# Optimization experiments

Hardware: AMD Instinct MI355X
Metric: run time of the kernel (lower is better)

Reference implementation:

```python
import jax, jax.numpy as jnp
import numpy as np

N, D, C = 4096, 512, 100000
S_SCALE, MARGIN = 30.0, 0.4


def setup_inputs() -> dict:
    key = jax.random.key(0)
    k1, k2, k3 = jax.random.split(key, 3)
    x = jax.random.normal(k1, (N, D), dtype=jnp.float32)
    labels = jax.random.randint(k2, (N,), 0, C, dtype=jnp.int64)
    # fc weight [out_features, in_features]; scaled so s*logits stays in fp32 exp range
    W = jax.random.normal(k3, (C, D), dtype=jnp.float32) * 0.02
    return {"x": x, "labels": labels, "W": W}


def reference(x, labels, W):
    # NOTE: the torch weight-normalization loop is a no-op (rebinds a local),
    # so W is used UNNORMALIZED, faithfully matching the executed torch math.
    xn = x / jnp.linalg.norm(x, axis=1, keepdims=True)          # F.normalize(x, dim=1)
    wf = jnp.einsum('nd,cd->nc', xn, W)                          # [N, C] logits
    target = jnp.take_along_axis(wf, labels[:, None], axis=1)[:, 0]  # wf[i, y_i]
    numerator = S_SCALE * (target - MARGIN)
    # sum over j != y_i of exp(s * wf[i, j]) without materializing per-row exclusions
    excl_sum = jnp.sum(jnp.exp(S_SCALE * wf), axis=1) - jnp.exp(S_SCALE * target)
    denominator = jnp.exp(numerator) + excl_sum
    L = numerator - jnp.log(denominator)
    return -jnp.mean(L)
```

## Files before the change

kernel.cpp:

```cpp
#include <hip/hip_runtime.h>

#define N_ROWS 4096
#define D_DIM  512
#define C_CLS  100000
#define S_SCALE 30.0f
#define MARGIN  0.4f

#define KS 16
#define NT 4
#define MTMAX 7
#define NBLK 1024
#define NTILES 6252
#define BASE_MT 6
#define EXTRA_T 108
#define LDS_BYTES (MTMAX * KS * 64 * 16)

typedef __attribute__((ext_vector_type(8))) __bf16 bf16x8;
typedef __attribute__((ext_vector_type(4))) float floatx4;

__device__ inline unsigned int f2bf_rne(float f) {
    unsigned int u = __builtin_bit_cast(unsigned int, f);
    u += 0x7fffu + ((u >> 16) & 1u);
    return u >> 16;
}

__device__ inline uint4 pack_bf16x8(float4 a, float4 b) {
    uint4 r;
    r.x = f2bf_rne(a.x) | (f2bf_rne(a.y) << 16);
    r.y = f2bf_rne(a.z) | (f2bf_rne(a.w) << 16);
    r.z = f2bf_rne(b.x) | (f2bf_rne(b.y) << 16);
    r.w = f2bf_rne(b.z) | (f2bf_rne(b.w) << 16);
    return r;
}

__global__ __launch_bounds__(256) void normalize_pack(
    const float* __restrict__ x, const int* __restrict__ labels,
    const float* __restrict__ W, uint4* __restrict__ xnp, float* __restrict__ target,
    float* __restrict__ row_sum)
{
    const int gt = blockIdx.x * 256 + threadIdx.x;
    if (gt < N_ROWS) row_sum[gt] = 0.f;

    const int lane = threadIdx.x & 63;
    const int r = blockIdx.x * 4 + (threadIdx.x >> 6);
    const float4* xr = (const float4*)(x + (size_t)r * D_DIM);
    float4 a = xr[lane * 2], b = xr[lane * 2 + 1];
    float ss = a.x*a.x + a.y*a.y + a.z*a.z + a.w*a.w
             + b.x*b.x + b.y*b.y + b.z*b.z + b.w*b.w;
    #pragma unroll
    for (int o = 1; o < 64; o <<= 1) ss += __shfl_xor(ss, o, 64);
    const float inv = 1.0f / sqrtf(ss);

    const int lab = labels[r];
    const float4* wr = (const float4*)(W + (size_t)lab * D_DIM);
    float4 wa = wr[lane * 2], wb = wr[lane * 2 + 1];
    float dot = a.x*wa.x + a.y*wa.y + a.z*wa.z + a.w*wa.w
              + b.x*wb.x + b.y*wb.y + b.z*wb.z + b.w*wb.w;
    #pragma unroll
    for (int o = 1; o < 64; o <<= 1) dot += __shfl_xor(dot, o, 64);
    if (lane == 0) target[r] = dot * inv;

    float4 na = {a.x*inv, a.y*inv, a.z*inv, a.w*inv};
    float4 nb = {b.x*inv, b.y*inv, b.z*inv, b.w*inv};
    const int nt = r >> 4, ks = lane >> 2, li = (r & 15) | ((lane & 3) << 4);
    xnp[(size_t)(nt * KS + ks) * 64 + li] = pack_bf16x8(na, nb);
}

__global__ __launch_bounds__(512, 2) void adms_main(
    const float* __restrict__ W, const uint4* __restrict__ xnp, float* __restrict__ row_sum)
{
    extern __shared__ uint4 sW[];
    const int tid = threadIdx.x, bid = blockIdx.x;
    const int tbase = bid * BASE_MT + (bid < EXTRA_T ? bid : EXTRA_T);
    const int cnt   = BASE_MT + (bid < EXTRA_T ? 1 : 0);
    const int c0 = tbase * 16;

    for (int g = tid >> 6; g < cnt * KS; g += 8) {
        const int mt = g >> 4, ks = g & 15;
        const int j8 = tid & 3, lm = (tid >> 2) & 15;
        const int gc = c0 + mt * 16 + lm;
        const int k0 = ks * 32 + j8 * 8;
        float4 v0 = {0.f,0.f,0.f,0.f}, v1 = {0.f,0.f,0.f,0.f};
        if (gc < C_CLS) {
            const float4* src = (const float4*)(W + (size_t)gc * D_DIM + k0);
            v0 = src[0]; v1 = src[1];
        }
        sW[(mt * KS + ks) * 64 + (lm | (j8 << 4))] = pack_bf16x8(v0, v1);
    }
    __syncthreads();

    const int w = tid >> 6, lane = tid & 63;
    const float s_log2e = S_SCALE * 1.44269504088896340736f;

    for (int iter = 0; iter < N_ROWS / 512; ++iter) {
        const int rbase = iter * 512 + w * 64;
        floatx4 acc[MTMAX][NT] = {};
        const size_t b0 = (size_t)(rbase >> 4) * (KS * 64) + lane;

        #pragma unroll 4
        for (int ks = 0; ks < KS; ++ks) {
            uint4 bfr[NT], afr[MTMAX];
            #pragma unroll
            for (int nt = 0; nt < NT; ++nt)
                bfr[nt] = xnp[b0 + (size_t)nt * (KS * 64) + ks * 64];
            #pragma unroll
            for (int mt = 0; mt < MTMAX; ++mt)
                if (mt < cnt) afr[mt] = sW[(mt * KS + ks) * 64 + lane];
            #pragma unroll
            for (int mt = 0; mt < MTMAX; ++mt)
                if (mt < cnt)
                    #pragma unroll
                    for (int nt = 0; nt < NT; ++nt)
                        acc[mt][nt] = __builtin_amdgcn_mfma_f32_16x16x32_bf16(
                            __builtin_bit_cast(bf16x8, afr[mt]),
                            __builtin_bit_cast(bf16x8, bfr[nt]),
                            acc[mt][nt], 0, 0, 0);
        }

        float rp[NT] = {0.f, 0.f, 0.f, 0.f};
        const int clsb = c0 + ((lane >> 4) << 2);
        #pragma unroll
        for (int mt = 0; mt < MTMAX; ++mt)
            if (mt < cnt)
                #pragma unroll
                for (int nt = 0; nt < NT; ++nt)
                    #pragma unroll
                    for (int r = 0; r < 4; ++r) {
                        const int cls = clsb + mt * 16 + r;
                        float e = (cls < C_CLS) ? exp2f(s_log2e * acc[mt][nt][r]) : 0.f;
                        rp[nt] += e;
                    }
        #pragma unroll
        for (int nt = 0; nt < NT; ++nt) {
            float v = rp[nt];
            v += __shfl_xor(v, 16, 64);
            v += __shfl_xor(v, 32, 64);
            if (lane < 16) atomicAdd(&row_sum[rbase + nt * 16 + lane], v);
        }
    }
}

__global__ __launch_bounds__(1024) void finalize(
    const float* __restrict__ target, const float* __restrict__ row_sum,
    float* __restrict__ out)
{
    __shared__ float red[1024];
    const int t = threadIdx.x;
    float accum = 0.f;
    for (int r = t; r < N_ROWS; r += 1024) {
        const float tg   = target[r];
        const float num  = S_SCALE * (tg - MARGIN);
        const float excl = row_sum[r] - expf(S_SCALE * tg);
        const float den  = expf(num) + excl;
        accum += num - logf(den);
    }
    red[t] = accum;
    __syncthreads();
    for (int s = 512; s > 0; s >>= 1) {
        if (t < s) red[t] += red[t + s];
        __syncthreads();
    }
    if (t == 0) out[0] = -red[0] / (float)N_ROWS;
}

extern "C" void kernel_launch(void* const* d_in, const int* in_sizes, int n_in,
                              void* d_out, int out_size, void* d_ws, size_t ws_size,
                              hipStream_t stream) {
    const float* x      = (const float*)d_in[0];
    const int*   labels = (const int*)d_in[1];
    const float* W      = (const float*)d_in[2];
    float* out = (float*)d_out;

    char* ws = (char*)d_ws;
    uint4* xnp     = (uint4*)ws;
    float* target  = (float*)(ws + (4u << 20));
    float* row_sum = (float*)(ws + (4u << 20) + (16u << 10));

    static bool attr_set = false;
    (void)attr_set;
    hipFuncSetAttribute((const void*)adms_main,
                        hipFuncAttributeMaxDynamicSharedMemorySize, LDS_BYTES);

    normalize_pack<<<N_ROWS / 4, 256, 0, stream>>>(x, labels, W, xnp, target, row_sum);
    adms_main<<<NBLK, 512, LDS_BYTES, stream>>>(W, xnp, row_sum);
    finalize<<<1, 1024, 0, stream>>>(target, row_sum, out);
}
```

Measured before the change: 660.3 us.

## Fold scale into normalized x, template tile count, rebalance blocks for occupancy

Pre-multiplies the normalized x by s*log2e so the MFMA output feeds the hardware exp2 directly. Specializes the main loop via a template on the per-block tile count, removing predicated tiles and class bounds checks, which works because the new split covers the classes exactly. Shrinks tiles per block and raises block count and launch-bound occupancy to cut register pressure and raise latency hiding. The trade-off is less reuse of each x fragment per block and more x traffic from cache.

```diff
diff --git a/kernel.cpp b/kernel.cpp
--- a/kernel.cpp
+++ b/kernel.cpp
@@ -8,12 +8,13 @@
 
 #define KS 16
 #define NT 4
-#define MTMAX 7
-#define NBLK 1024
-#define NTILES 6252
-#define BASE_MT 6
-#define EXTRA_T 108
+#define MTMAX 5
+#define NBLK 1536
+#define BASE_MT 4
+#define EXTRA_T 106
 #define LDS_BYTES (MTMAX * KS * 64 * 16)
+
+#define S_LOG2E 43.2808512266689f
 
 typedef __attribute__((ext_vector_type(8))) __bf16 bf16x8;
 typedef __attribute__((ext_vector_type(4))) float floatx4;
@@ -60,13 +61,61 @@
     for (int o = 1; o < 64; o <<= 1) dot += __shfl_xor(dot, o, 64);
     if (lane == 0) target[r] = dot * inv;
 
-    float4 na = {a.x*inv, a.y*inv, a.z*inv, a.w*inv};
-    float4 nb = {b.x*inv, b.y*inv, b.z*inv, b.w*inv};
+    const float invs = inv * S_LOG2E;
+    float4 na = {a.x*invs, a.y*invs, a.z*invs, a.w*invs};
+    float4 nb = {b.x*invs, b.y*invs, b.z*invs, b.w*invs};
     const int nt = r >> 4, ks = lane >> 2, li = (r & 15) | ((lane & 3) << 4);
     xnp[(size_t)(nt * KS + ks) * 64 + li] = pack_bf16x8(na, nb);
 }
 
-__global__ __launch_bounds__(512, 2) void adms_main(
+template<int CNT>
+__device__ __forceinline__ void run_stripe(
+    const uint4* __restrict__ xnp, const uint4* __restrict__ sW,
+    float* __restrict__ row_sum, int w, int lane)
+{
+    for (int iter = 0; iter < N_ROWS / 512; ++iter) {
+        const int rbase = iter * 512 + w * 64;
+        floatx4 acc[CNT][NT] = {};
+        const int b0 = (rbase >> 4) * (KS * 64) + lane;
+
+        #pragma unroll 2
+        for (int ks = 0; ks < KS; ++ks) {
+            uint4 bfr[NT], afr[CNT];
+            #pragma unroll
+            for (int nt = 0; nt < NT; ++nt)
+                bfr[nt] = xnp[b0 + nt * (KS * 64) + ks * 64];
+            #pragma unroll
+            for (int mt = 0; mt < CNT; ++mt)
+                afr[mt] = sW[(mt * KS + ks) * 64 + lane];
+            #pragma unroll
+            for (int mt = 0; mt < CNT; ++mt)
+                #pragma unroll
+                for (int nt = 0; nt < NT; ++nt)
+                    acc[mt][nt] = __builtin_amdgcn_mfma_f32_16x16x32_bf16(
+                        __builtin_bit_cast(bf16x8, afr[mt]),
+                        __builtin_bit_cast(bf16x8, bfr[nt]),
+                        acc[mt][nt], 0, 0, 0);
+        }
+
+        float rp[NT] = {0.f, 0.f, 0.f, 0.f};
+        #pragma unroll
+        for (int mt = 0; mt < CNT; ++mt)
+            #pragma unroll
+            for (int nt = 0; nt < NT; ++nt)
+                #pragma unroll
+                for (int r = 0; r < 4; ++r)
+                    rp[nt] += __builtin_amdgcn_exp2f(acc[mt][nt][r]);
+        #pragma unroll
+        for (int nt = 0; nt < NT; ++nt) {
+            float v = rp[nt];
+            v += __shfl_xor(v, 16, 64);
+            v += __shfl_xor(v, 32, 64);
+            if (lane < 16) atomicAdd(&row_sum[rbase + nt * 16 + lane], v);
+        }
+    }
+}
+
+__global__ __launch_bounds__(512, 4) void adms_main(
     const float* __restrict__ W, const uint4* __restrict__ xnp, float* __restrict__ row_sum)
 {
     extern __shared__ uint4 sW[];
@@ -80,64 +129,14 @@
         const int j8 = tid & 3, lm = (tid >> 2) & 15;
         const int gc = c0 + mt * 16 + lm;
         const int k0 = ks * 32 + j8 * 8;
-        float4 v0 = {0.f,0.f,0.f,0.f}, v1 = {0.f,0.f,0.f,0.f};
-        if (gc < C_CLS) {
-            const float4* src = (const float4*)(W + (size_t)gc * D_DIM + k0);
-            v0 = src[0]; v1 = src[1];
-        }
-        sW[(mt * KS + ks) * 64 + (lm | (j8 << 4))] = pack_bf16x8(v0, v1);
+        const float4* src = (const float4*)(W + (size_t)gc * D_DIM + k0);
+        sW[(mt * KS + ks) * 64 + (lm | (j8 << 4))] = pack_bf16x8(src[0], src[1]);
     }
     __syncthreads();
 
     const int w = tid >> 6, lane = tid & 63;
-    const float s_log2e = S_SCALE * 1.44269504088896340736f;
-
-    for (int iter = 0; iter < N_ROWS / 512; ++iter) {
-        const int rbase = iter * 512 + w * 64;
-        floatx4 acc[MTMAX][NT] = {};
-        const size_t b0 = (size_t)(rbase >> 4) * (KS * 64) + lane;
-
-        #pragma unroll 4
-        for (int ks = 0; ks < KS; ++ks) {
-            uint4 bfr[NT], afr[MTMAX];
-            #pragma unroll
-            for (int nt = 0; nt < NT; ++nt)
-                bfr[nt] = xnp[b0 + (size_t)nt * (KS * 64) + ks * 64];
-            #pragma unroll
-            for (int mt = 0; mt < MTMAX; ++mt)
-                if (mt < cnt) afr[mt] = sW[(mt * KS + ks) * 64 + lane];
-            #pragma unroll
-            for (int mt = 0; mt < MTMAX; ++mt)
-                if (mt < cnt)
-                    #pragma unroll
-                    for (int nt = 0; nt < NT; ++nt)
-                        acc[mt][nt] = __builtin_amdgcn_mfma_f32_16x16x32_bf16(
-                            __builtin_bit_cast(bf16x8, afr[mt]),
-                            __builtin_bit_cast(bf16x8, bfr[nt]),
-                            acc[mt][nt], 0, 0, 0);
-        }
-
-        float rp[NT] = {0.f, 0.f, 0.f, 0.f};
-        const int clsb = c0 + ((lane >> 4) << 2);
-        #pragma unroll
-        for (int mt = 0; mt < MTMAX; ++mt)
-            if (mt < cnt)
-                #pragma unroll
-                for (int nt = 0; nt < NT; ++nt)
-                    #pragma unroll
-                    for (int r = 0; r < 4; ++r) {
-                        const int cls = clsb + mt * 16 + r;
-                        float e = (cls < C_CLS) ? exp2f(s_log2e * acc[mt][nt][r]) : 0.f;
-                        rp[nt] += e;
-                    }
-        #pragma unroll
-        for (int nt = 0; nt < NT; ++nt) {
-            float v = rp[nt];
-            v += __shfl_xor(v, 16, 64);
-            v += __shfl_xor(v, 32, 64);
-            if (lane < 16) atomicAdd(&row_sum[rbase + nt * 16 + lane], v);
-        }
-    }
+    if (cnt == 5) run_stripe<5>(xnp, sW, row_sum, w, lane);
+    else          run_stripe<4>(xnp, sW, row_sum, w, lane);
 }
 
 __global__ __launch_bounds__(1024) void finalize(
@@ -176,8 +175,6 @@
     float* target  = (float*)(ws + (4u << 20));
     float* row_sum = (float*)(ws + (4u << 20) + (16u << 10));
 
-    static bool attr_set = false;
-    (void)attr_set;
     hipFuncSetAttribute((const void*)adms_main,
                         hipFuncAttributeMaxDynamicSharedMemorySize, LDS_BYTES);
 
```

Measured after the change: 627.8 us. -4.9%, faster.
